# Performance work log

Measured on AMD Instinct MI355X. Metric: run time of the kernel, lower is better.

## Reference

```python
import jax, jax.numpy as jnp
from jax import lax
import numpy as np

K = 9  # 3x3 kernel taps


def _mdconv(x, w, off_w, off_b):
    # Modulated deformable conv v2, kernel 3x3, stride 1, pad 1, no bias.
    N, C, H, W = x.shape
    # offset/mask predictor: plain 3x3 conv -> 27 channels (18 offsets + 9 mask)
    off = lax.conv_general_dilated(x, off_w, (1, 1), ((1, 1), (1, 1))) + off_b[None, :, None, None]
    o = off[:, :2 * K].reshape(N, K, 2, H, W)  # channel 2k = dy_k, 2k+1 = dx_k
    dy, dx = o[:, :, 0], o[:, :, 1]            # [N,K,H,W]
    m = jax.nn.sigmoid(off[:, 2 * K:])          # modulation mask [N,K,H,W]
    ky = jnp.arange(K) // 3 - 1                 # kernel tap row offsets
    kx = jnp.arange(K) % 3 - 1
    py = dy + ky[None, :, None, None] + jnp.arange(H)[None, None, :, None]
    px = dx + kx[None, :, None, None] + jnp.arange(W)[None, None, None, :]
    y0 = jnp.floor(py)
    x0 = jnp.floor(px)
    ly = py - y0
    lx = px - x0
    y0i = y0.astype(jnp.int32)
    x0i = x0.astype(jnp.int32)
    x_flat = x.reshape(N, C, H * W)

    def corner(yi, xi, wgt):
        valid = (yi >= 0) & (yi < H) & (xi >= 0) & (xi < W)  # zero padding outside
        idx = jnp.clip(yi, 0, H - 1) * W + jnp.clip(xi, 0, W - 1)  # [N,K,H,W]
        g = jax.vmap(lambda xf, ix: xf[:, ix.reshape(-1)])(x_flat, idx)
        g = g.reshape(N, C, K, H, W)
        return g * (wgt * valid)[:, None]

    s = (corner(y0i, x0i, (1 - ly) * (1 - lx))
         + corner(y0i, x0i + 1, (1 - ly) * lx)
         + corner(y0i + 1, x0i, ly * (1 - lx))
         + corner(y0i + 1, x0i + 1, ly * lx))
    s = s * m[:, None]  # modulate sampled values
    return jnp.einsum('nckhw,ock->nohw', s, w.reshape(w.shape[0], C, K))


def _bn_relu(x, g, b, eps=1e-5):
    # training-mode BatchNorm2d (batch statistics over N,H,W) + ReLU
    mu = x.mean((0, 2, 3), keepdims=True)
    var = ((x - mu) ** 2).mean((0, 2, 3), keepdims=True)
    return jax.nn.relu((x - mu) * lax.rsqrt(var + eps) * g[None, :, None, None] + b[None, :, None, None])


def setup_inputs() -> dict:
    key = jax.random.key(0)
    ks = jax.random.split(key, 5)
    N, Cin, Cmid, Cout, H, W = 4, 64, 128, 128, 96, 96
    x = jax.random.normal(ks[0], (N, Cin, H, W), jnp.float32)
    w1 = jax.random.normal(ks[1], (Cmid, Cin, 3, 3), jnp.float32) * 0.06   # ~kaiming scale
    w2 = jax.random.normal(ks[2], (Cout, Cmid, 3, 3), jnp.float32) * 0.04
    off_w1 = jax.random.normal(ks[3], (27, Cin, 3, 3), jnp.float32) * 0.01  # small offsets
    off_w2 = jax.random.normal(ks[4], (27, Cmid, 3, 3), jnp.float32) * 0.01
    return {
        'x': x,
        'w1': w1, 'off_w1': off_w1, 'off_b1': jnp.zeros((27,), jnp.float32),
        'gamma1': jnp.ones((Cmid,), jnp.float32), 'beta1': jnp.zeros((Cmid,), jnp.float32),
        'w2': w2, 'off_w2': off_w2, 'off_b2': jnp.zeros((27,), jnp.float32),
        'gamma2': jnp.ones((Cout,), jnp.float32), 'beta2': jnp.zeros((Cout,), jnp.float32),
    }


def reference(x, w1, off_w1, off_b1, gamma1, beta1, w2, off_w2, off_b2, gamma2, beta2):
    h = _bn_relu(_mdconv(x, w1, off_w1, off_b1), gamma1, beta1)
    return _bn_relu(_mdconv(h, w2, off_w2, off_b2), gamma2, beta2)
```

## Files before the change

### kernel.cpp

```cpp
#include <hip/hip_runtime.h>
#include <math.h>

#define N_  4
#define H_  96
#define W_  96
#define HW  9216
#define NHW 36864
#define O_  128
#define PW  98
#define PHW 9604

typedef unsigned short ushort_t;
typedef __attribute__((ext_vector_type(8))) short bf16x8;
typedef __attribute__((ext_vector_type(4))) float f32x4;
typedef __attribute__((ext_vector_type(8))) unsigned short u16x8;

__device__ __forceinline__ float bf2f(ushort_t u) {
  return __uint_as_float(((unsigned int)u) << 16);
}
__device__ __forceinline__ ushort_t f2bf(float f) {
  unsigned int u = __float_as_uint(f);
  u += 0x7fffu + ((u >> 16) & 1u);
  return (ushort_t)(u >> 16);
}

__global__ __launch_bounds__(256) void to_nhwc_pad_kernel(const float* __restrict__ x,
                                                          ushort_t* __restrict__ xp, int C) {
  __shared__ ushort_t L[32][33];
  int ctiles = C >> 5;
  int b = blockIdx.x;
  int ct = b % ctiles;
  int hwt = (b / ctiles) % (HW / 32);
  int n = b / (ctiles * (HW / 32));
  int tx = threadIdx.x & 31, ty = threadIdx.x >> 5;
#pragma unroll
  for (int i = 0; i < 4; ++i) {
    int cl = ty + i * 8;
    L[cl][tx] = f2bf(x[((size_t)(n * C + ct * 32 + cl)) * HW + hwt * 32 + tx]);
  }
  __syncthreads();
#pragma unroll
  for (int i = 0; i < 4; ++i) {
    int hl = ty + i * 8;
    int hw = hwt * 32 + hl;
    int y = hw / W_, xx = hw % W_;
    xp[((size_t)n * PHW + (y + 1) * PW + (xx + 1)) * C + ct * 32 + tx] = L[tx][hl];
  }
}

__global__ void transpose_w_kernel(const float* __restrict__ w,
                                   ushort_t* __restrict__ wB, int C) {
  int K = C * 9;
  int i = blockIdx.x * 256 + threadIdx.x;
  if (i >= 128 * K) return;
  int o = i / K, r = i % K;
  int kk = r / C, c = r % C;
  wB[i] = f2bf(w[(o * C + c) * 9 + kk]);
}

__global__ void transpose_wo_kernel(const float* __restrict__ ow,
                                    ushort_t* __restrict__ wOB, int C) {
  int K = C * 9;
  int i = blockIdx.x * 256 + threadIdx.x;
  if (i >= 32 * K) return;
  int o = i / K, r = i % K;
  int kk = r / C, c = r % C;
  wOB[i] = (o < 27) ? f2bf(ow[(o * C + c) * 9 + kk]) : (ushort_t)0;
}

__device__ __forceinline__ void gll16(const ushort_t* g, ushort_t* l) {
  __builtin_amdgcn_global_load_lds((const __attribute__((address_space(1))) void*)g,
                                   (__attribute__((address_space(3))) void*)l, 16, 0, 0);
}
__device__ __forceinline__ int swz(int row) {
  return (row & 3) ^ ((row >> 2) & 3);
}

template <int C>
__global__ __launch_bounds__(256) void gemm_off_kernel(
    const ushort_t* __restrict__ xp, const ushort_t* __restrict__ B,
    const float* __restrict__ ob, float* __restrict__ offt) {
  constexpr int K = C * 9;
  __shared__ __align__(16) ushort_t As[64 * 32];
  __shared__ __align__(16) ushort_t Bs[32 * 32];
  int tid = threadIdx.x;
  int m0 = blockIdx.x * 64;
  int lane = tid & 63, wid = tid >> 6;
  f32x4 acc[2];
  acc[0] = (f32x4){0.f, 0.f, 0.f, 0.f};
  acc[1] = (f32x4){0.f, 0.f, 0.f, 0.f};
  int srow = tid >> 2, chl = tid & 3, q = lane >> 4;
  int mg = m0 + srow;
  int nl = mg / HW, hw = mg % HW;
  int y = hw / W_, x = hw % W_;
  const ushort_t* xn = xp + (size_t)nl * PHW * C;
  int pbase = ((y + 1) * PW + (x + 1)) * C;
  int chg = chl ^ swz(srow);
  for (int kt = 0; kt < K; kt += 32) {
    int kk = kt / C, c0 = kt % C;
    int shift = ((kk / 3 - 1) * PW + (kk % 3 - 1)) * C;
    gll16(xn + pbase + shift + c0 + chg * 8, As + tid * 8);
    if (tid < 128) {
      int row = tid >> 2;
      gll16(B + (size_t)row * K + kt + ((tid & 3) ^ swz(row)) * 8, Bs + tid * 8);
    }
    __syncthreads();
    int r = wid * 16 + (lane & 15);
    bf16x8 af = *reinterpret_cast<const bf16x8*>(&As[r * 32 + ((q ^ swz(r)) << 3)]);
#pragma unroll
    for (int oi = 0; oi < 2; ++oi) {
      int rb = oi * 16 + (lane & 15);
      bf16x8 bfr = *reinterpret_cast<const bf16x8*>(&Bs[rb * 32 + ((q ^ swz(rb)) << 3)]);
      acc[oi] = __builtin_amdgcn_mfma_f32_16x16x32_bf16(af, bfr, acc[oi], 0, 0, 0);
    }
    __syncthreads();
  }
#pragma unroll
  for (int oi = 0; oi < 2; ++oi) {
    int o = oi * 16 + (lane & 15);
    if (o < 27) {
      float b = ob[o];
      int mb = m0 + wid * 16 + ((lane >> 4) << 2);
#pragma unroll
      for (int j = 0; j < 4; ++j)
        offt[(size_t)(mb + j) * 28 + o] = acc[oi][j] + b;
    }
  }
}

template <int C>
__global__ __launch_bounds__(256) void gemm_fused_kernel(
    const ushort_t* __restrict__ xp, const float* __restrict__ offt,
    const ushort_t* __restrict__ B, float* __restrict__ Y,
    float* __restrict__ stats) {
  constexpr int K = C * 9;
  __shared__ __align__(16) ushort_t As[64 * 32];
  __shared__ __align__(16) ushort_t Bs[128 * 32];
  int tid = threadIdx.x;
  int m0 = blockIdx.x * 64;
  int lane = tid & 63, wid = tid >> 6;
  int wr = wid >> 1, wc = wid & 1;
  f32x4 acc[2][4];
#pragma unroll
  for (int mi = 0; mi < 2; ++mi)
#pragma unroll
    for (int oi = 0; oi < 4; ++oi) acc[mi][oi] = (f32x4){0.f, 0.f, 0.f, 0.f};
  int srow = tid >> 2, chl = tid & 3, q = lane >> 4;
  int mg = m0 + srow;
  int n = mg / HW, hw = mg % HW;
  int h = hw / W_, w = hw % W_;
  const float* op = offt + (size_t)mg * 28;
  const ushort_t* xb = xp + (size_t)n * PHW * C;
  const ushort_t *p00 = xb, *p01 = xb, *p10 = xb, *p11 = xb;
  float w00 = 0.f, w01 = 0.f, w10 = 0.f, w11 = 0.f;
  int wslot = (chl ^ swz(srow)) << 3;

  for (int kt = 0; kt < K; kt += 32) {
    int kk = kt / C, c0 = kt % C;
    if (c0 == 0) {
      float dy = op[2 * kk], dx = op[2 * kk + 1], mo = op[18 + kk];
      float mm = 1.f / (1.f + __expf(-mo));
      float py = dy + (float)(kk / 3 - 1 + h);
      float px = dx + (float)(kk % 3 - 1 + w);
      float fy = floorf(py), fx = floorf(px);
      int y0 = (int)fy, x0 = (int)fx;
      float ly = py - fy, lx = px - fx;
      int y1 = y0 + 1, x1 = x0 + 1;
      bool vy0 = (y0 >= 0) & (y0 < H_), vy1 = (y1 >= 0) & (y1 < H_);
      bool vx0 = (x0 >= 0) & (x0 < W_), vx1 = (x1 >= 0) & (x1 < W_);
      int y0c = min(max(y0, 0), H_ - 1), y1c = min(max(y1, 0), H_ - 1);
      int x0c = min(max(x0, 0), W_ - 1), x1c = min(max(x1, 0), W_ - 1);
      w00 = (vy0 & vx0) ? (1.f - ly) * (1.f - lx) * mm : 0.f;
      w01 = (vy0 & vx1) ? (1.f - ly) * lx * mm : 0.f;
      w10 = (vy1 & vx0) ? ly * (1.f - lx) * mm : 0.f;
      w11 = (vy1 & vx1) ? ly * lx * mm : 0.f;
      p00 = xb + (size_t)((y0c + 1) * PW + x0c + 1) * C;
      p01 = xb + (size_t)((y0c + 1) * PW + x1c + 1) * C;
      p10 = xb + (size_t)((y1c + 1) * PW + x0c + 1) * C;
      p11 = xb + (size_t)((y1c + 1) * PW + x1c + 1) * C;
    }
#pragma unroll
    for (int rr = 0; rr < 2; ++rr) {
      int row = srow + 64 * rr;
      gll16(B + (size_t)row * K + kt + ((chl ^ swz(row)) << 3), Bs + rr * 2048 + tid * 8);
    }
    int c = c0 + chl * 8;
    u16x8 va = *reinterpret_cast<const u16x8*>(p00 + c);
    u16x8 vb = *reinterpret_cast<const u16x8*>(p01 + c);
    u16x8 vc = *reinterpret_cast<const u16x8*>(p10 + c);
    u16x8 vd = *reinterpret_cast<const u16x8*>(p11 + c);
    u16x8 r;
#pragma unroll
    for (int e = 0; e < 8; ++e) {
      float v = w00 * bf2f(va[e]) + w01 * bf2f(vb[e])
              + w10 * bf2f(vc[e]) + w11 * bf2f(vd[e]);
      r[e] = f2bf(v);
    }
    *reinterpret_cast<u16x8*>(&As[srow * 32 + wslot]) = r;
    __syncthreads();
    bf16x8 af[2], bfr[4];
#pragma unroll
    for (int mi = 0; mi < 2; ++mi) {
      int rr2 = wr * 32 + mi * 16 + (lane & 15);
      af[mi] = *reinterpret_cast<const bf16x8*>(&As[rr2 * 32 + ((q ^ swz(rr2)) << 3)]);
    }
#pragma unroll
    for (int oi = 0; oi < 4; ++oi) {
      int rr2 = wc * 64 + oi * 16 + (lane & 15);
      bfr[oi] = *reinterpret_cast<const bf16x8*>(&Bs[rr2 * 32 + ((q ^ swz(rr2)) << 3)]);
    }
#pragma unroll
    for (int mi = 0; mi < 2; ++mi)
#pragma unroll
      for (int oi = 0; oi < 4; ++oi)
        acc[mi][oi] = __builtin_amdgcn_mfma_f32_16x16x32_bf16(af[mi], bfr[oi], acc[mi][oi], 0, 0, 0);
    __syncthreads();
  }
#pragma unroll
  for (int mi = 0; mi < 2; ++mi)
#pragma unroll
    for (int oi = 0; oi < 4; ++oi) {
      int o = wc * 64 + oi * 16 + (lane & 15);
      int mb = m0 + wr * 32 + mi * 16 + ((lane >> 4) << 2);
#pragma unroll
      for (int j = 0; j < 4; ++j)
        Y[(size_t)(mb + j) * O_ + o] = acc[mi][oi][j];
    }
#pragma unroll
  for (int oi = 0; oi < 4; ++oi) {
    float s = 0.f, s2 = 0.f;
#pragma unroll
    for (int mi = 0; mi < 2; ++mi)
#pragma unroll
      for (int j = 0; j < 4; ++j) {
        float v = acc[mi][oi][j];
        s += v; s2 += v * v;
      }
    s  += __shfl_xor(s, 16);  s  += __shfl_xor(s, 32);
    s2 += __shfl_xor(s2, 16); s2 += __shfl_xor(s2, 32);
    if ((lane >> 4) == 0) {
      int o = wc * 64 + oi * 16 + (lane & 15);
      atomicAdd(&stats[o], s);
      atomicAdd(&stats[128 + o], s2);
    }
  }
}

__global__ __launch_bounds__(256) void bn_apply_pad_kernel(
    const float* __restrict__ Y, const float* __restrict__ stats,
    const float* __restrict__ gamma, const float* __restrict__ beta,
    ushort_t* __restrict__ hp) {
  int g = blockIdx.x * 256 + threadIdx.x;
  int m = g >> 4;
  int o0 = (g & 15) * 8;
  int n = m / HW, hw = m % HW;
  int y = hw / W_, x = hw % W_;
  const float4* yp = reinterpret_cast<const float4*>(Y) + (size_t)g * 2;
  float4 a = yp[0], b = yp[1];
  float va[8] = {a.x, a.y, a.z, a.w, b.x, b.y, b.z, b.w};
  u16x8 r;
#pragma unroll
  for (int e = 0; e < 8; ++e) {
    int o = o0 + e;
    float mu = stats[o] * (1.f / (float)NHW);
    float var = stats[128 + o] * (1.f / (float)NHW) - mu * mu;
    float sc = rsqrtf(var + 1e-5f) * gamma[o];
    float sh = beta[o] - mu * sc;
    r[e] = f2bf(fmaxf(fmaf(va[e], sc, sh), 0.f));
  }
  size_t pp = ((size_t)n * PHW + (y + 1) * PW + (x + 1)) * 128;
  *reinterpret_cast<u16x8*>(hp + pp + o0) = r;
}

__global__ __launch_bounds__(256) void bn_apply_t_kernel(
    const float* __restrict__ Y, const float* __restrict__ stats,
    const float* __restrict__ gamma, const float* __restrict__ beta,
    float* __restrict__ outf) {
  __shared__ float L[64][129];
  __shared__ float Lsc[128], Lsh[128];
  int tid = threadIdx.x;
  int m0 = blockIdx.x * 64;
  if (tid < 128) {
    float mu = stats[tid] * (1.f / (float)NHW);
    float var = stats[128 + tid] * (1.f / (float)NHW) - mu * mu;
    float sc = rsqrtf(var + 1e-5f) * gamma[tid];
    Lsc[tid] = sc;
    Lsh[tid] = beta[tid] - mu * sc;
  }
#pragma unroll
  for (int it = 0; it < 8; ++it) {
    int idx = it * 256 + tid;
    int ml = idx >> 5, oq = idx & 31;
    float4 v = *reinterpret_cast<const float4*>(&Y[(size_t)(m0 + ml) * O_ + oq * 4]);
    L[ml][oq * 4 + 0] = v.x; L[ml][oq * 4 + 1] = v.y;
    L[ml][oq * 4 + 2] = v.z; L[ml][oq * 4 + 3] = v.w;
  }
  __syncthreads();
  int n = m0 / HW, hw0 = m0 % HW;
#pragma unroll
  for (int it = 0; it < 32; ++it) {
    int idx = it * 256 + tid;
    int ol = idx >> 6, ml = idx & 63;
    float r = fmaxf(fmaf(L[ml][ol], Lsc[ol], Lsh[ol]), 0.f);
    outf[((size_t)n * O_ + ol) * HW + hw0 + ml] = r;
  }
}

extern "C" void kernel_launch(void* const* d_in, const int* in_sizes, int n_in,
                              void* d_out, int out_size, void* d_ws, size_t ws_size,
                              hipStream_t stream) {
  const float* x      = (const float*)d_in[0];
  const float* w1     = (const float*)d_in[1];
  const float* off_w1 = (const float*)d_in[2];
  const float* off_b1 = (const float*)d_in[3];
  const float* gamma1 = (const float*)d_in[4];
  const float* beta1  = (const float*)d_in[5];
  const float* w2     = (const float*)d_in[6];
  const float* off_w2 = (const float*)d_in[7];
  const float* off_b2 = (const float*)d_in[8];
  const float* gamma2 = (const float*)d_in[9];
  const float* beta2  = (const float*)d_in[10];
  float* out = (float*)d_out;

  char* p = (char*)d_ws;
  auto alloc = [&](size_t bytes) -> void* {
    void* r = (void*)p;
    p += (bytes + 255) & ~(size_t)255;
    return r;
  };
  float*    offt  = (float*)alloc((size_t)NHW * 28 * 4);
  float*    Y     = (float*)alloc((size_t)NHW * O_ * 4);
  float*    stats = (float*)alloc(512 * 4);
  ushort_t* wB1   = (ushort_t*)alloc(73728 * 2);
  ushort_t* wB2   = (ushort_t*)alloc(147456 * 2);
  ushort_t* wOB1  = (ushort_t*)alloc(32 * 576 * 2);
  ushort_t* wOB2  = (ushort_t*)alloc(32 * 1152 * 2);
  ushort_t* xp    = (ushort_t*)alloc((size_t)N_ * PHW * 64 * 2);
  ushort_t* hp    = (ushort_t*)alloc((size_t)N_ * PHW * 128 * 2);

  hipMemsetAsync(xp, 0, (size_t)N_ * PHW * (64 + 128) * 2, stream);
  hipMemsetAsync(stats, 0, 512 * 4, stream);
  to_nhwc_pad_kernel<<<2304, 256, 0, stream>>>(x, xp, 64);
  transpose_w_kernel<<<288, 256, 0, stream>>>(w1, wB1, 64);
  transpose_w_kernel<<<576, 256, 0, stream>>>(w2, wB2, 128);
  transpose_wo_kernel<<<72, 256, 0, stream>>>(off_w1, wOB1, 64);
  transpose_wo_kernel<<<144, 256, 0, stream>>>(off_w2, wOB2, 128);

  gemm_off_kernel<64><<<576, 256, 0, stream>>>(xp, wOB1, off_b1, offt);
  gemm_fused_kernel<64><<<576, 256, 0, stream>>>(xp, offt, wB1, Y, stats);
  bn_apply_pad_kernel<<<2304, 256, 0, stream>>>(Y, stats, gamma1, beta1, hp);

  gemm_off_kernel<128><<<576, 256, 0, stream>>>(hp, wOB2, off_b2, offt);
  gemm_fused_kernel<128><<<576, 256, 0, stream>>>(hp, offt, wB2, Y, stats + 256);
  bn_apply_t_kernel<<<576, 256, 0, stream>>>(Y, stats + 256, gamma2, beta2, out);
}
```

Measured before the change: 258.4 us.

## Widen fused deform-GEMM K-tile to 64 and use 8 waves per block

The fused sampling+GEMM kernel now processes 64 K-elements per iteration instead of 32 and launches 512 threads (8 waves) per block, with each wave computing a 32x32 output tile instead of 32x64. This halves the number of barrier-separated iterations and doubles the number of threads doing the bilinear gather per tile, aiming to hide gather latency and cut sync overhead. The costs are doubled LDS per block, fewer accumulators per wave, and a new XOR swizzle over 8 slots.

```diff
diff --git a/kernel.cpp b/kernel.cpp
--- a/kernel.cpp
+++ b/kernel.cpp
@@ -129,23 +129,25 @@
 }
 
 template <int C>
-__global__ __launch_bounds__(256) void gemm_fused_kernel(
+__global__ __launch_bounds__(512) void gemm_fused_kernel(
     const ushort_t* __restrict__ xp, const float* __restrict__ offt,
     const ushort_t* __restrict__ B, float* __restrict__ Y,
     float* __restrict__ stats) {
   constexpr int K = C * 9;
-  __shared__ __align__(16) ushort_t As[64 * 32];
-  __shared__ __align__(16) ushort_t Bs[128 * 32];
+  __shared__ __align__(16) ushort_t As[64 * 64];
+  __shared__ __align__(16) ushort_t Bs[128 * 64];
   int tid = threadIdx.x;
   int m0 = blockIdx.x * 64;
   int lane = tid & 63, wid = tid >> 6;
-  int wr = wid >> 1, wc = wid & 1;
-  f32x4 acc[2][4];
+  int wr = wid >> 2, wc = wid & 3;
+  f32x4 acc[2][2];
 #pragma unroll
   for (int mi = 0; mi < 2; ++mi)
 #pragma unroll
-    for (int oi = 0; oi < 4; ++oi) acc[mi][oi] = (f32x4){0.f, 0.f, 0.f, 0.f};
-  int srow = tid >> 2, chl = tid & 3, q = lane >> 4;
+    for (int oi = 0; oi < 2; ++oi) acc[mi][oi] = (f32x4){0.f, 0.f, 0.f, 0.f};
+  int srow = tid >> 3;
+  int sl = tid & 7;
+  int q = lane >> 4;
   int mg = m0 + srow;
   int n = mg / HW, hw = mg % HW;
   int h = hw / W_, w = hw % W_;
@@ -153,9 +155,9 @@
   const ushort_t* xb = xp + (size_t)n * PHW * C;
   const ushort_t *p00 = xb, *p01 = xb, *p10 = xb, *p11 = xb;
   float w00 = 0.f, w01 = 0.f, w10 = 0.f, w11 = 0.f;
-  int wslot = (chl ^ swz(srow)) << 3;
-
-  for (int kt = 0; kt < K; kt += 32) {
+  int wpos = (sl ^ (srow & 7)) << 3;
+
+  for (int kt = 0; kt < K; kt += 64) {
     int kk = kt / C, c0 = kt % C;
     if (c0 == 0) {
       float dy = op[2 * kk], dx = op[2 * kk + 1], mo = op[18 + kk];
@@ -181,10 +183,11 @@
     }
 #pragma unroll
     for (int rr = 0; rr < 2; ++rr) {
-      int row = srow + 64 * rr;
-      gll16(B + (size_t)row * K + kt + ((chl ^ swz(row)) << 3), Bs + rr * 2048 + tid * 8);
-    }
-    int c = c0 + chl * 8;
+      int row = rr * 64 + srow;
+      gll16(B + (size_t)row * K + kt + ((sl ^ (row & 7)) << 3),
+            Bs + (rr * 512 + tid) * 8);
+    }
+    int c = c0 + sl * 8;
     u16x8 va = *reinterpret_cast<const u16x8*>(p00 + c);
     u16x8 vb = *reinterpret_cast<const u16x8*>(p01 + c);
     u16x8 vc = *reinterpret_cast<const u16x8*>(p10 + c);
@@ -196,38 +199,47 @@
               + w10 * bf2f(vc[e]) + w11 * bf2f(vd[e]);
       r[e] = f2bf(v);
     }
-    *reinterpret_cast<u16x8*>(&As[srow * 32 + wslot]) = r;
+    *reinterpret_cast<u16x8*>(&As[srow * 64 + wpos]) = r;
     __syncthreads();
-    bf16x8 af[2], bfr[4];
+    bf16x8 af[2][2], bfr[2][2];
 #pragma unroll
     for (int mi = 0; mi < 2; ++mi) {
-      int rr2 = wr * 32 + mi * 16 + (lane & 15);
-      af[mi] = *reinterpret_cast<const bf16x8*>(&As[rr2 * 32 + ((q ^ swz(rr2)) << 3)]);
-    }
-#pragma unroll
-    for (int oi = 0; oi < 4; ++oi) {
-      int rr2 = wc * 64 + oi * 16 + (lane & 15);
-      bfr[oi] = *reinterpret_cast<const bf16x8*>(&Bs[rr2 * 32 + ((q ^ swz(rr2)) << 3)]);
-    }
-#pragma unroll
-    for (int mi = 0; mi < 2; ++mi)
-#pragma unroll
-      for (int oi = 0; oi < 4; ++oi)
-        acc[mi][oi] = __builtin_amdgcn_mfma_f32_16x16x32_bf16(af[mi], bfr[oi], acc[mi][oi], 0, 0, 0);
+      int rA = wr * 32 + mi * 16 + (lane & 15);
+#pragma unroll
+      for (int ks = 0; ks < 2; ++ks)
+        af[mi][ks] = *reinterpret_cast<const bf16x8*>(
+            &As[rA * 64 + (((ks * 4 + q) ^ (rA & 7)) << 3)]);
+    }
+#pragma unroll
+    for (int oi = 0; oi < 2; ++oi) {
+      int rB = wc * 32 + oi * 16 + (lane & 15);
+#pragma unroll
+      for (int ks = 0; ks < 2; ++ks)
+        bfr[oi][ks] = *reinterpret_cast<const bf16x8*>(
+            &Bs[rB * 64 + (((ks * 4 + q) ^ (rB & 7)) << 3)]);
+    }
+#pragma unroll
+    for (int ks = 0; ks < 2; ++ks)
+#pragma unroll
+      for (int mi = 0; mi < 2; ++mi)
+#pragma unroll
+        for (int oi = 0; oi < 2; ++oi)
+          acc[mi][oi] = __builtin_amdgcn_mfma_f32_16x16x32_bf16(
+              af[mi][ks], bfr[oi][ks], acc[mi][oi], 0, 0, 0);
     __syncthreads();
   }
 #pragma unroll
   for (int mi = 0; mi < 2; ++mi)
 #pragma unroll
-    for (int oi = 0; oi < 4; ++oi) {
-      int o = wc * 64 + oi * 16 + (lane & 15);
+    for (int oi = 0; oi < 2; ++oi) {
+      int o = wc * 32 + oi * 16 + (lane & 15);
       int mb = m0 + wr * 32 + mi * 16 + ((lane >> 4) << 2);
 #pragma unroll
       for (int j = 0; j < 4; ++j)
         Y[(size_t)(mb + j) * O_ + o] = acc[mi][oi][j];
     }
 #pragma unroll
-  for (int oi = 0; oi < 4; ++oi) {
+  for (int oi = 0; oi < 2; ++oi) {
     float s = 0.f, s2 = 0.f;
 #pragma unroll
     for (int mi = 0; mi < 2; ++mi)
@@ -239,7 +251,7 @@
     s  += __shfl_xor(s, 16);  s  += __shfl_xor(s, 32);
     s2 += __shfl_xor(s2, 16); s2 += __shfl_xor(s2, 32);
     if ((lane >> 4) == 0) {
-      int o = wc * 64 + oi * 16 + (lane & 15);
+      int o = wc * 32 + oi * 16 + (lane & 15);
       atomicAdd(&stats[o], s);
       atomicAdd(&stats[128 + o], s2);
     }
@@ -347,10 +359,10 @@
   transpose_wo_kernel<<<144, 256, 0, stream>>>(off_w2, wOB2, 128);
 
   gemm_off_kernel<64><<<576, 256, 0, stream>>>(xp, wOB1, off_b1, offt);
-  gemm_fused_kernel<64><<<576, 256, 0, stream>>>(xp, offt, wB1, Y, stats);
+  gemm_fused_kernel<64><<<576, 512, 0, stream>>>(xp, offt, wB1, Y, stats);
   bn_apply_pad_kernel<<<2304, 256, 0, stream>>>(Y, stats, gamma1, beta1, hp);
 
   gemm_off_kernel<128><<<576, 256, 0, stream>>>(hp, wOB2, off_b2, offt);
-  gemm_fused_kernel<128><<<576, 256, 0, stream>>>(hp, offt, wB2, Y, stats + 256);
+  gemm_fused_kernel<128><<<576, 512, 0, stream>>>(hp, offt, wB2, Y, stats + 256);
   bn_apply_t_kernel<<<576, 256, 0, stream>>>(Y, stats + 256, gamma2, beta2, out);
 }
```

After: 250.4 us. -3.1%, faster.
